# Performance work log

Hardware: AMD Instinct MI355X
Metric: run time of the kernel (lower is better)

Reference implementation:

```python
import jax, jax.numpy as jnp
import numpy as np

B = 2048   # batch
D = 1280   # backbone feature dim (hardcoded in module)
E = 8      # num_classes == number of expert heads
ALPHA = 0.1
EPS = 1e-5


def _bn(x, g, b, m, v):
    # BatchNorm1d in eval mode: running stats
    return (x - m) * jax.lax.rsqrt(v + EPS) * g + b


def _ln(x, g, b):
    mu = jnp.mean(x, axis=-1, keepdims=True)
    var = jnp.mean((x - mu) ** 2, axis=-1, keepdims=True)
    return (x - mu) * jax.lax.rsqrt(var + EPS) * g + b


@jax.custom_vjp
def _grad_reverse(x):
    return x

def _gr_fwd(x):
    return x, None

def _gr_bwd(_, g):
    return (-ALPHA * g,)

_grad_reverse.defvjp(_gr_fwd, _gr_bwd)


def setup_inputs() -> dict:
    key = jax.random.key(0)
    ks = iter(jax.random.split(key, 80))
    def w(*s):
        return jax.random.normal(next(ks), s, dtype=jnp.float32) * 0.02
    def u(*s):
        return jax.random.uniform(next(ks), s, dtype=jnp.float32) + 0.5
    inp = {"source": jax.random.normal(next(ks), (B, D), dtype=jnp.float32)}
    # bottleneck: Linear(1280,512)+BN+ReLU, Linear(512,256)+BN+ReLU
    inp.update(bw1=w(D, 512), bb1=jnp.zeros(512), bg1=jnp.ones(512), bbe1=jnp.zeros(512), bm1=w(512), bv1=u(512))
    inp.update(bw2=w(512, 256), bb2=jnp.zeros(256), bg2=jnp.ones(256), bbe2=jnp.zeros(256), bm2=w(256), bv2=u(256))
    # source_fc: Linear(256, E) + LogSoftmax
    inp.update(cw=w(256, E), cb=jnp.zeros(E))
    # domain classifier: 1280->1024->1024->512->2 with BN
    inp.update(dw1=w(D, 1024), db1=jnp.zeros(1024), dg1=jnp.ones(1024), dbe1=jnp.zeros(1024), dm1=w(1024), dv1=u(1024))
    inp.update(dw2=w(1024, 1024), db2=jnp.zeros(1024), dg2=jnp.ones(1024), dbe2=jnp.zeros(1024), dm2=w(1024), dv2=u(1024))
    inp.update(dw3=w(1024, 512), db3=jnp.zeros(512), dg3=jnp.ones(512), dbe3=jnp.zeros(512), dm3=w(512), dv3=u(512))
    inp.update(dw4=w(512, 2), db4=jnp.zeros(2))
    # E stacked expert MLPs: 1280->1024->1024->512->2 with LayerNorm
    inp.update(ew1=w(E, D, 1024), eb1=jnp.zeros((E, 1024)), eg1=jnp.ones((E, 1024)), ebe1=jnp.zeros((E, 1024)))
    inp.update(ew2=w(E, 1024, 1024), eb2=jnp.zeros((E, 1024)), eg2=jnp.ones((E, 1024)), ebe2=jnp.zeros((E, 1024)))
    inp.update(ew3=w(E, 1024, 512), eb3=jnp.zeros((E, 512)), eg3=jnp.ones((E, 512)), ebe3=jnp.zeros((E, 512)))
    inp.update(ew4=w(E, 512, 2), eb4=jnp.zeros((E, 2)))
    return inp


def reference(source, bw1, bb1, bg1, bbe1, bm1, bv1, bw2, bb2, bg2, bbe2, bm2, bv2, cw, cb,
              dw1, db1, dg1, dbe1, dm1, dv1, dw2, db2, dg2, dbe2, dm2, dv2,
              dw3, db3, dg3, dbe3, dm3, dv3, dw4, db4,
              ew1, eb1, eg1, ebe1, ew2, eb2, eg2, ebe2, ew3, eb3, eg3, ebe3, ew4, eb4):
    share = source  # sharedNet modeled as identity on extracted features
    # bottleneck + classifier head
    h = jax.nn.relu(_bn(share @ bw1 + bb1, bg1, bbe1, bm1, bv1))
    h = jax.nn.relu(_bn(h @ bw2 + bb2, bg2, bbe2, bm2, bv2))
    src = jax.nn.log_softmax(h @ cw + cb, axis=-1)            # [B, E]
    label = jnp.argmax(src, axis=-1)                          # routing labels (detached by argmax)
    # gradient-reversed features
    rev = _grad_reverse(share)
    # global domain classifier (dropout = identity in eval)
    d = jax.nn.relu(_bn(rev @ dw1 + db1, dg1, dbe1, dm1, dv1))
    d = jax.nn.relu(_bn(d @ dw2 + db2, dg2, dbe2, dm2, dv2))
    d = jax.nn.relu(_bn(d @ dw3 + db3, dg3, dbe3, dm3, dv3))
    dclf = jax.nn.log_softmax(d @ dw4 + db4, axis=-1)         # [B, 2]
    # per-class domain experts: dense all-expert compute + per-sample gather
    x = jax.nn.relu(_ln(jnp.einsum('bd,edh->beh', rev, ew1) + eb1[None], eg1[None], ebe1[None]))
    x = jax.nn.relu(_ln(jnp.einsum('beh,ehk->bek', x, ew2) + eb2[None], eg2[None], ebe2[None]))
    x = jax.nn.relu(_ln(jnp.einsum('beh,ehk->bek', x, ew3) + eb3[None], eg3[None], ebe3[None]))
    eo = jax.nn.log_softmax(jnp.einsum('beh,ehk->bek', x, ew4) + eb4[None], axis=-1)  # [B, E, 2]
    sout = jnp.take_along_axis(eo, label[:, None, None], axis=1)[:, 0, :]             # [B, 2]
    return (src, dclf, sout, share)
```

## Files before the change

kernel.cpp:

```cpp
#include <hip/hip_runtime.h>

typedef unsigned short u16;
typedef short s8v __attribute__((ext_vector_type(8)));
typedef float f4v __attribute__((ext_vector_type(4)));

#define AS1 __attribute__((address_space(1)))
#define AS3 __attribute__((address_space(3)))

__device__ __forceinline__ float bf2f(u16 u) {
    union { unsigned int i; float f; } x; x.i = ((unsigned int)u) << 16; return x.f;
}
__device__ __forceinline__ u16 f2bf(float f) {
    union { float f; unsigned int i; } x; x.f = f;
    unsigned int r = x.i + 0x7fffu + ((x.i >> 16) & 1u);
    return (u16)(r >> 16);
}

__device__ __forceinline__ void glds16(const u16* g, u16* l) {
    __builtin_amdgcn_global_load_lds((AS1 void*)(g), (AS3 void*)(l), 16, 0, 0);
}

__device__ __forceinline__ int swz(int row, int kq) {
    return row * 64 + ((((kq >> 3) ^ row) & 7) << 3);
}

__global__ __launch_bounds__(256) void convT2_k(const float* __restrict__ Wa,
        const float* __restrict__ Wb, int zSplit,
        u16* __restrict__ WT, int N, int K)
{
    const int z = blockIdx.z;
    const float* W = (z < zSplit) ? Wa + (size_t)z * K * N
                                  : Wb + (size_t)(z - zSplit) * K * N;
    WT += (size_t)z * K * N;
    const int n0 = blockIdx.x * 64, k0 = blockIdx.y * 64;
    __shared__ float t[64][65];
    const int r = threadIdx.x >> 2;
    const int c = (threadIdx.x & 3) << 4;
    const float* wp = W + (size_t)(k0 + r) * N + n0 + c;
    #pragma unroll
    for (int q = 0; q < 16; q += 4) {
        float4 f = *(const float4*)(wp + q);
        t[c + q + 0][r] = f.x; t[c + q + 1][r] = f.y;
        t[c + q + 2][r] = f.z; t[c + q + 3][r] = f.w;
    }
    __syncthreads();
    u16* op = WT + (size_t)(n0 + r) * K + k0 + c;
    #pragma unroll
    for (int q = 0; q < 16; q += 8) {
        s8v v;
        #pragma unroll
        for (int j = 0; j < 8; ++j) v[j] = (short)f2bf(t[r][c + q + j]);
        *(s8v*)(op + q) = v;
    }
}

__global__ __launch_bounds__(256) void conv_k(const float* __restrict__ in,
        u16* __restrict__ out, int n8)
{
    const int i = blockIdx.x * 256 + threadIdx.x;
    if (i >= n8) return;
    const float4 f0 = ((const float4*)in)[i * 2];
    const float4 f1 = ((const float4*)in)[i * 2 + 1];
    s8v v;
    v[0]=(short)f2bf(f0.x); v[1]=(short)f2bf(f0.y);
    v[2]=(short)f2bf(f0.z); v[3]=(short)f2bf(f0.w);
    v[4]=(short)f2bf(f1.x); v[5]=(short)f2bf(f1.y);
    v[6]=(short)f2bf(f1.z); v[7]=(short)f2bf(f1.w);
    ((s8v*)out)[i] = v;
}

__device__ __forceinline__ void stage_tile(u16* AsH, u16* BsH,
        const u16* ga, const u16* gb, int kk, int ldsq, int K)
{
    #pragma unroll
    for (int q = 0; q < 4; ++q) {
        glds16(ga + kk + (size_t)q * 32 * K, AsH + q * 2048 + ldsq);
        glds16(gb + kk + (size_t)q * 32 * K, BsH + q * 2048 + ldsq);
    }
}

template<int HASDOM>
__global__ __launch_bounds__(256) void gemm_bt128_k(
    const u16* __restrict__ A0, size_t aStrideZ,
    const u16* __restrict__ WT0,
    const float* __restrict__ ebias,
    const float* __restrict__ dbias, const float* __restrict__ dgam,
    const float* __restrict__ dbet,  const float* __restrict__ dmean,
    const float* __restrict__ dvar,  int zdom,
    u16* __restrict__ out0, int M, int N, int K)
{
    const int z = blockIdx.z;
    const u16* A  = A0  + (size_t)z * aStrideZ;
    const u16* WT = WT0 + (size_t)z * N * K;
    u16* out = out0 + (size_t)z * M * N;

    const int n0 = blockIdx.x * 128, m0 = blockIdx.y * 128;
    const int t = threadIdx.x;
    const int w = t >> 6, lane = t & 63;
    const int lq = lane >> 4, lr = lane & 15;
    const int wm = (w >> 1) * 64, wn = (w & 1) * 64;

    __shared__ __align__(16) u16 As[2 * 128 * 64];
    __shared__ __align__(16) u16 Bs[2 * 128 * 64];

    f4v acc[4][4] = {};

    const int schunk = ((t & 7) ^ ((t >> 3) & 7)) << 3;
    const u16* ga = A  + (size_t)(m0 + (t >> 3)) * K + schunk;
    const u16* gb = WT + (size_t)(n0 + (t >> 3)) * K + schunk;
    const int ldsq = w * 512;

    const int NT = K >> 6;
    int cur = 0;
    stage_tile(As, Bs, ga, gb, 0, ldsq, K);
    __syncthreads();

    for (int tk = 0; tk < NT; ++tk) {
        if (tk + 1 < NT)
            stage_tile(As + (cur ^ 1) * 8192, Bs + (cur ^ 1) * 8192,
                       ga, gb, (tk + 1) << 6, ldsq, K);
        const u16* Ah = As + cur * 8192;
        const u16* Bh = Bs + cur * 8192;
        __builtin_amdgcn_s_setprio(1);
        #pragma unroll
        for (int ks = 0; ks < 64; ks += 32) {
            const int kq = ks + (lq << 3);
            s8v a[4], b[4];
            #pragma unroll
            for (int i = 0; i < 4; ++i) a[i] = *(const s8v*)&Ah[swz(wm + i*16 + lr, kq)];
            #pragma unroll
            for (int j = 0; j < 4; ++j) b[j] = *(const s8v*)&Bh[swz(wn + j*16 + lr, kq)];
            #pragma unroll
            for (int i = 0; i < 4; ++i)
                #pragma unroll
                for (int j = 0; j < 4; ++j)
                    acc[i][j] = __builtin_amdgcn_mfma_f32_16x16x32_bf16(a[i], b[j], acc[i][j], 0, 0, 0);
        }
        __builtin_amdgcn_s_setprio(0);
        __syncthreads();
        cur ^= 1;
    }

    float scale[4], shift[4];
    const bool dom = HASDOM && (z == zdom);
    #pragma unroll
    for (int j = 0; j < 4; ++j) {
        const int c = n0 + wn + j * 16 + lr;
        if (dom) {
            const float s = dgam[c] / sqrtf(dvar[c] + 1e-5f);
            scale[j] = s;
            shift[j] = (dbias[c] - dmean[c]) * s + dbet[c];
        } else {
            scale[j] = 1.f;
            shift[j] = ebias[(size_t)z * N + c];
        }
    }
    const int r0 = lq << 2;
    #pragma unroll
    for (int i = 0; i < 4; ++i) {
        #pragma unroll
        for (int r = 0; r < 4; ++r) {
            const int grow = m0 + wm + i * 16 + r0 + r;
            u16* orow = out + (size_t)grow * N + n0 + wn + lr;
            #pragma unroll
            for (int j = 0; j < 4; ++j) {
                float y = fmaf(acc[i][j][r], scale[j], shift[j]);
                if (dom) y = fmaxf(y, 0.f);
                orow[j * 16] = f2bf(y);
            }
        }
    }
}

__global__ __launch_bounds__(256) void gemm_f32sk_k(
    const float* __restrict__ A, const float* __restrict__ W,
    float* __restrict__ out, int M, int N, int K, int Ks)
{
    const int n0 = blockIdx.x * 64, m0 = blockIdx.y * 64;
    const int kb = blockIdx.z * Ks;
    out += (size_t)blockIdx.z * M * N;
    const int tid = threadIdx.x;
    const int tx = tid & 15, ty = tid >> 4;
    __shared__ float As[64][65];
    __shared__ float Bs[64][64];
    float acc[4][4] = {};
    const int sr = tid >> 2;
    const int sc = (tid & 3) << 4;
    for (int kk = kb; kk < kb + Ks; kk += 64) {
        const float* ap = A + (size_t)(m0 + sr) * K + kk + sc;
        #pragma unroll
        for (int q = 0; q < 4; ++q) {
            float4 f = *(const float4*)(ap + q * 4);
            As[sr][sc + q*4 + 0] = f.x; As[sr][sc + q*4 + 1] = f.y;
            As[sr][sc + q*4 + 2] = f.z; As[sr][sc + q*4 + 3] = f.w;
        }
        const float* wp = W + (size_t)(kk + sr) * N + n0 + sc;
        #pragma unroll
        for (int q = 0; q < 4; ++q)
            *(float4*)&Bs[sr][sc + q*4] = *(const float4*)(wp + q * 4);
        __syncthreads();
        #pragma unroll 4
        for (int kq = 0; kq < 64; ++kq) {
            float a[4], bv[4];
            #pragma unroll
            for (int i = 0; i < 4; ++i) a[i] = As[ty*4 + i][kq];
            #pragma unroll
            for (int j = 0; j < 4; ++j) bv[j] = Bs[kq][tx*4 + j];
            #pragma unroll
            for (int i = 0; i < 4; ++i)
                #pragma unroll
                for (int j = 0; j < 4; ++j)
                    acc[i][j] = fmaf(a[i], bv[j], acc[i][j]);
        }
        __syncthreads();
    }
    #pragma unroll
    for (int j = 0; j < 4; ++j) {
        const int c = n0 + tx*4 + j;
        #pragma unroll
        for (int i = 0; i < 4; ++i)
            out[(size_t)(m0 + ty*4 + i) * N + c] = acc[i][j];
    }
}

__global__ __launch_bounds__(256) void h2cls_k(
    const float* __restrict__ hp,
    const float* __restrict__ bb1, const float* __restrict__ bg1,
    const float* __restrict__ bbe1, const float* __restrict__ bm1,
    const float* __restrict__ bv1,
    const float* __restrict__ bw2, const float* __restrict__ bb2,
    const float* __restrict__ bg2, const float* __restrict__ bbe2,
    const float* __restrict__ bm2, const float* __restrict__ bv2,
    const float* __restrict__ cw,  const float* __restrict__ cb,
    float* __restrict__ out_src, int* __restrict__ label, int B)
{
    const int b0 = blockIdx.x * 4;
    const int t = threadIdx.x;
    const size_t sl = (size_t)B * 512;
    __shared__ float h1s[4][512];
    __shared__ float h2s[4][256];

    #pragma unroll
    for (int cc = 0; cc < 2; ++cc) {
        const int c = t + cc * 256;
        const float sc = bg1[c] / sqrtf(bv1[c] + 1e-5f);
        const float sh = (bb1[c] - bm1[c]) * sc + bbe1[c];
        #pragma unroll
        for (int s = 0; s < 4; ++s) {
            const size_t ix = (size_t)(b0 + s) * 512 + c;
            const float v = hp[ix] + hp[ix + sl] + hp[ix + 2*sl] + hp[ix + 3*sl];
            h1s[s][c] = fmaxf(fmaf(v, sc, sh), 0.f);
        }
    }
    __syncthreads();

    float acc[4] = {};
    #pragma unroll 4
    for (int k = 0; k < 512; ++k) {
        const float wv = bw2[(size_t)k * 256 + t];
        #pragma unroll
        for (int s = 0; s < 4; ++s) acc[s] = fmaf(h1s[s][k], wv, acc[s]);
    }
    const float sc2 = bg2[t] / sqrtf(bv2[t] + 1e-5f);
    const float sh2 = (bb2[t] - bm2[t]) * sc2 + bbe2[t];
    #pragma unroll
    for (int s = 0; s < 4; ++s) h2s[s][t] = fmaxf(fmaf(acc[s], sc2, sh2), 0.f);
    __syncthreads();

    const int s = t >> 6, lane = t & 63;
    float p[8] = {};
    for (int k = lane; k < 256; k += 64) {
        const float x = h2s[s][k];
        #pragma unroll
        for (int c = 0; c < 8; ++c) p[c] = fmaf(x, cw[k * 8 + c], p[c]);
    }
    #pragma unroll
    for (int off = 32; off; off >>= 1)
        #pragma unroll
        for (int c = 0; c < 8; ++c) p[c] += __shfl_xor(p[c], off, 64);
    if (lane == 0) {
        const int b = b0 + s;
        float lg[8];
        #pragma unroll
        for (int c = 0; c < 8; ++c) lg[c] = p[c] + cb[c];
        float mx = lg[0]; int am = 0;
        #pragma unroll
        for (int c = 1; c < 8; ++c) if (lg[c] > mx) { mx = lg[c]; am = c; }
        float ssum = 0.f;
        #pragma unroll
        for (int c = 0; c < 8; ++c) ssum += expf(lg[c] - mx);
        const float lse = mx + logf(ssum);
        #pragma unroll
        for (int c = 0; c < 8; ++c) out_src[b * 8 + c] = lg[c] - lse;
        label[b] = am;
    }
}

template<int N>
__global__ __launch_bounds__(256) void ln_relu_k(u16* __restrict__ Y,
        const float* __restrict__ g, const float* __restrict__ bb)
{
    const int z = blockIdx.y;
    u16* y = Y + ((size_t)z * gridDim.x + blockIdx.x) * N;
    const float* gz = g  + (size_t)z * N;
    const float* bz = bb + (size_t)z * N;
    const int t = threadIdx.x;
    constexpr int C = N >> 8;
    float vals[C];
    if (C == 4) {
        ushort4 u = ((const ushort4*)y)[t];
        vals[0] = bf2f(u.x); vals[1] = bf2f(u.y);
        vals[2] = bf2f(u.z); vals[3] = bf2f(u.w);
    } else {
        ushort2 u = ((const ushort2*)y)[t];
        vals[0] = bf2f(u.x); vals[1] = bf2f(u.y);
    }
    float s = 0.f, sq = 0.f;
    #pragma unroll
    for (int i = 0; i < C; ++i) { s += vals[i]; sq += vals[i] * vals[i]; }
    #pragma unroll
    for (int off = 32; off; off >>= 1) {
        s  += __shfl_xor(s,  off, 64);
        sq += __shfl_xor(sq, off, 64);
    }
    __shared__ float rs[4], rq[4];
    if ((t & 63) == 0) { rs[t >> 6] = s; rq[t >> 6] = sq; }
    __syncthreads();
    s  = rs[0] + rs[1] + rs[2] + rs[3];
    sq = rq[0] + rq[1] + rq[2] + rq[3];
    const float inv = 1.f / (float)N;
    const float mu  = s * inv;
    const float var = sq * inv - mu * mu;
    const float rstd = rsqrtf(var + 1e-5f);
    if (C == 4) {
        float4 gv = ((const float4*)gz)[t];
        float4 bv = ((const float4*)bz)[t];
        ushort4 o;
        o.x = f2bf(fmaxf((vals[0] - mu) * rstd * gv.x + bv.x, 0.f));
        o.y = f2bf(fmaxf((vals[1] - mu) * rstd * gv.y + bv.y, 0.f));
        o.z = f2bf(fmaxf((vals[2] - mu) * rstd * gv.z + bv.z, 0.f));
        o.w = f2bf(fmaxf((vals[3] - mu) * rstd * gv.w + bv.w, 0.f));
        ((ushort4*)y)[t] = o;
    } else {
        float2 gv = ((const float2*)gz)[t];
        float2 bv = ((const float2*)bz)[t];
        ushort2 o;
        o.x = f2bf(fmaxf((vals[0] - mu) * rstd * gv.x + bv.x, 0.f));
        o.y = f2bf(fmaxf((vals[1] - mu) * rstd * gv.y + bv.y, 0.f));
        ((ushort2*)y)[t] = o;
    }
}

__global__ __launch_bounds__(64) void head2_k(const u16* __restrict__ X, size_t xsz,
        const float* __restrict__ W, size_t wsz,
        const float* __restrict__ bias, size_t bsz,
        int K, float* __restrict__ out, size_t osz)
{
    const int b = blockIdx.x, z = blockIdx.y;
    const int lane = threadIdx.x;
    const u16* x = X + z * xsz + (size_t)b * K;
    const float* Wz = W + z * wsz;
    const float* bz = bias + z * bsz;
    float* o = out + z * osz + (size_t)b * 2;
    float p0 = 0.f, p1 = 0.f;
    for (int k = lane; k < K; k += 64) {
        const float xv = bf2f(x[k]);
        p0 = fmaf(xv, Wz[k * 2],     p0);
        p1 = fmaf(xv, Wz[k * 2 + 1], p1);
    }
    #pragma unroll
    for (int off = 32; off; off >>= 1) {
        p0 += __shfl_xor(p0, off, 64);
        p1 += __shfl_xor(p1, off, 64);
    }
    if (lane == 0) {
        const float l0 = p0 + bz[0];
        const float l1 = p1 + bz[1];
        const float mx = fmaxf(l0, l1);
        const float lse = mx + logf(expf(l0 - mx) + expf(l1 - mx));
        o[0] = l0 - lse;
        o[1] = l1 - lse;
    }
}

__global__ __launch_bounds__(256) void gather_k(const float* __restrict__ eo,
        const int* __restrict__ label, float* __restrict__ out, int B)
{
    const int b = blockIdx.x * 256 + threadIdx.x;
    if (b >= B) return;
    const int e = label[b];
    out[b * 2]     = eo[((size_t)e * B + b) * 2];
    out[b * 2 + 1] = eo[((size_t)e * B + b) * 2 + 1];
}

__global__ __launch_bounds__(256) void copy16_k(const uint4* __restrict__ in,
                                                uint4* __restrict__ out, int n16)
{
    const int i = blockIdx.x * blockDim.x + threadIdx.x;
    if (i < n16) out[i] = in[i];
}


extern "C" void kernel_launch(void* const* d_in, const int* in_sizes, int n_in,
                              void* d_out, int out_size, void* d_ws, size_t ws_size,
                              hipStream_t stream)
{
    const int B = 2048, D = 1280, E = 8;

    const float* src = (const float*)d_in[0];
    const float *bw1 = (const float*)d_in[1],  *bb1 = (const float*)d_in[2],
                *bg1 = (const float*)d_in[3],  *bbe1 = (const float*)d_in[4],
                *bm1 = (const float*)d_in[5],  *bv1 = (const float*)d_in[6];
    const float *bw2 = (const float*)d_in[7],  *bb2 = (const float*)d_in[8],
                *bg2 = (const float*)d_in[9],  *bbe2 = (const float*)d_in[10],
                *bm2 = (const float*)d_in[11], *bv2 = (const float*)d_in[12];
    const float *cw  = (const float*)d_in[13], *cb  = (const float*)d_in[14];
    const float *dw1 = (const float*)d_in[15], *db1 = (const float*)d_in[16],
                *dg1 = (const float*)d_in[17], *dbe1 = (const float*)d_in[18],
                *dm1 = (const float*)d_in[19], *dv1 = (const float*)d_in[20];
    const float *dw2 = (const float*)d_in[21], *db2 = (const float*)d_in[22],
                *dg2 = (const float*)d_in[23], *dbe2 = (const float*)d_in[24],
                *dm2 = (const float*)d_in[25], *dv2 = (const float*)d_in[26];
    const float *dw3 = (const float*)d_in[27], *db3 = (const float*)d_in[28],
                *dg3 = (const float*)d_in[29], *dbe3 = (const float*)d_in[30],
                *dm3 = (const float*)d_in[31], *dv3 = (const float*)d_in[32];
    const float *dw4 = (const float*)d_in[33], *db4 = (const float*)d_in[34];
    const float *ew1 = (const float*)d_in[35], *eb1 = (const float*)d_in[36],
                *eg1 = (const float*)d_in[37], *ebe1 = (const float*)d_in[38];
    const float *ew2 = (const float*)d_in[39], *eb2 = (const float*)d_in[40],
                *eg2 = (const float*)d_in[41], *ebe2 = (const float*)d_in[42];
    const float *ew3 = (const float*)d_in[43], *eb3 = (const float*)d_in[44],
                *eg3 = (const float*)d_in[45], *ebe3 = (const float*)d_in[46];
    const float *ew4 = (const float*)d_in[47], *eb4 = (const float*)d_in[48];

    float* out_src   = (float*)d_out;
    float* out_dclf  = out_src + B * E;
    float* out_sout  = out_dclf + B * 2;
    float* out_share = out_sout + B * 2;

    char* ws = (char*)d_ws;
    u16*   wslot = (u16*)ws;
    u16*   srcb  = (u16*)(ws + 13107200);
    u16*   acta  = (u16*)(ws + 18350080);
    u16*   actb  = (u16*)(ws + 39321600);
    float* eo    = (float*)(ws + 60293120);
    int*   label = (int*)(ws + 60424192);
    float* hp    = (float*)(ws + 18350080);

    const size_t s1024 = (size_t)B * 1024, s512 = (size_t)B * 512;

    conv_k<<<dim3(B * D / 8 / 256), 256, 0, stream>>>(src, srcb, B * D / 8);
    copy16_k<<<dim3(B * D * 4 / 16 / 256), 256, 0, stream>>>(
        (const uint4*)src, (uint4*)out_share, B * D * 4 / 16);

    gemm_f32sk_k<<<dim3(512 / 64, B / 64, 4), 256, 0, stream>>>(
        src, bw1, hp, B, 512, D, 320);
    h2cls_k<<<dim3(B / 4), 256, 0, stream>>>(
        hp, bb1, bg1, bbe1, bm1, bv1, bw2, bb2, bg2, bbe2, bm2, bv2,
        cw, cb, out_src, label, B);

    convT2_k<<<dim3(16, 20, 5), 256, 0, stream>>>(ew1, dw1, 4, wslot, 1024, 1280);
    gemm_bt128_k<1><<<dim3(8, 16, 5), 256, 0, stream>>>(
        srcb, 0, wslot, eb1, db1, dg1, dbe1, dm1, dv1, 4, acta, B, 1024, 1280);
    ln_relu_k<1024><<<dim3(B, 4), 256, 0, stream>>>(acta, eg1, ebe1);

    convT2_k<<<dim3(16, 16, 5), 256, 0, stream>>>(ew2, dw2, 4, wslot, 1024, 1024);
    gemm_bt128_k<1><<<dim3(8, 16, 5), 256, 0, stream>>>(
        acta, s1024, wslot, eb2, db2, dg2, dbe2, dm2, dv2, 4, actb, B, 1024, 1024);
    ln_relu_k<1024><<<dim3(B, 4), 256, 0, stream>>>(actb, eg2, ebe2);

    convT2_k<<<dim3(8, 16, 5), 256, 0, stream>>>(ew3, dw3, 4, wslot, 512, 1024);
    gemm_bt128_k<1><<<dim3(4, 16, 5), 256, 0, stream>>>(
        actb, s1024, wslot, eb3, db3, dg3, dbe3, dm3, dv3, 4, acta, B, 512, 1024);
    ln_relu_k<512><<<dim3(B, 4), 256, 0, stream>>>(acta, eg3, ebe3);

    head2_k<<<dim3(B, 4), 64, 0, stream>>>(
        acta, s512, ew4, 1024, eb4, 2, 512, eo, (size_t)B * 2);
    head2_k<<<dim3(B, 1), 64, 0, stream>>>(
        acta + (size_t)4 * B * 512, 0, dw4, 0, db4, 0, 512, out_dclf, 0);

    convT2_k<<<dim3(16, 20, 4), 256, 0, stream>>>(
        ew1 + (size_t)4*1280*1024, ew1 + (size_t)4*1280*1024, 4, wslot, 1024, 1280);
    gemm_bt128_k<0><<<dim3(8, 16, 4), 256, 0, stream>>>(
        srcb, 0, wslot, eb1 + (size_t)4*1024,
        nullptr, nullptr, nullptr, nullptr, nullptr, -1, acta, B, 1024, 1280);
    ln_relu_k<1024><<<dim3(B, 4), 256, 0, stream>>>(acta, eg1 + (size_t)4*1024, ebe1 + (size_t)4*1024);

    convT2_k<<<dim3(16, 16, 4), 256, 0, stream>>>(
        ew2 + (size_t)4*1024*1024, ew2 + (size_t)4*1024*1024, 4, wslot, 1024, 1024);
    gemm_bt128_k<0><<<dim3(8, 16, 4), 256, 0, stream>>>(
        acta, s1024, wslot, eb2 + (size_t)4*1024,
        nullptr, nullptr, nullptr, nullptr, nullptr, -1, actb, B, 1024, 1024);
    ln_relu_k<1024><<<dim3(B, 4), 256, 0, stream>>>(actb, eg2 + (size_t)4*1024, ebe2 + (size_t)4*1024);

    convT2_k<<<dim3(8, 16, 4), 256, 0, stream>>>(
        ew3 + (size_t)4*1024*512, ew3 + (size_t)4*1024*512, 4, wslot, 512, 1024);
    gemm_bt128_k<0><<<dim3(4, 16, 4), 256, 0, stream>>>(
        actb, s1024, wslot, eb3 + (size_t)4*512,
        nullptr, nullptr, nullptr, nullptr, nullptr, -1, acta, B, 512, 1024);
    ln_relu_k<512><<<dim3(B, 4), 256, 0, stream>>>(acta, eg3 + (size_t)4*512, ebe3 + (size_t)4*512);

    head2_k<<<dim3(B, 4), 64, 0, stream>>>(
        acta, s512, ew4 + (size_t)4*512*2, 1024, eb4 + 8, 2, 512,
        eo + (size_t)4 * B * 2, (size_t)B * 2);

    gather_k<<<dim3(B / 256), 256, 0, stream>>>(eo, label, out_sout, B);
}
```

Baseline: 620.9 us.

## Split bottleneck layer-2 into tiled split-K GEMM plus classifier kernel; vectorize head loads

The fused h2cls kernel, which ran the 512->256 bottleneck matmul with only 4 rows per block, is replaced by three kernels. A tiny kernel precomputes the BN1 scale and shift. A 64x64 tiled split-K GEMM applies BN1+ReLU while staging activations into shared memory, which gives far more weight reuse. A classifier kernel reduces the split-K partials, applies BN2+ReLU and computes log-softmax/argmax. The expert head kernel also loads activations and weights with 16-byte vector loads; the cost is two extra launches and a partial-sum buffer round trip through global memory.

```diff
diff --git a/kernel.cpp b/kernel.cpp
--- a/kernel.cpp
+++ b/kernel.cpp
@@ -223,63 +223,125 @@
     }
 }
 
-__global__ __launch_bounds__(256) void h2cls_k(
-    const float* __restrict__ hp,
-    const float* __restrict__ bb1, const float* __restrict__ bg1,
-    const float* __restrict__ bbe1, const float* __restrict__ bm1,
-    const float* __restrict__ bv1,
-    const float* __restrict__ bw2, const float* __restrict__ bb2,
+__global__ __launch_bounds__(256) void bnpre_k(const float* __restrict__ g,
+        const float* __restrict__ be, const float* __restrict__ bb,
+        const float* __restrict__ m, const float* __restrict__ v,
+        float* __restrict__ scs, float* __restrict__ shs, int N)
+{
+    const int k = blockIdx.x * 256 + threadIdx.x;
+    if (k >= N) return;
+    const float sc = g[k] / sqrtf(v[k] + 1e-5f);
+    scs[k] = sc;
+    shs[k] = (bb[k] - m[k]) * sc + be[k];
+}
+
+__global__ __launch_bounds__(256) void h2gemm_k(
+    const float* __restrict__ hp, const float* __restrict__ scs,
+    const float* __restrict__ shs, const float* __restrict__ bw2,
+    float* __restrict__ out, int B)
+{
+    const int n0 = blockIdx.x * 64, m0 = blockIdx.y * 64;
+    const int kb = blockIdx.z * 128;
+    out += (size_t)blockIdx.z * B * 256;
+    const size_t sl = (size_t)B * 512;
+    const int tid = threadIdx.x;
+    const int tx = tid & 15, ty = tid >> 4;
+    __shared__ float As[64][65];
+    __shared__ float Bs[64][64];
+    float acc[4][4] = {};
+    const int sr = tid >> 2;
+    const int sc = (tid & 3) << 4;
+    for (int kk = kb; kk < kb + 128; kk += 64) {
+        const float* ap = hp + (size_t)(m0 + sr) * 512 + kk + sc;
+        #pragma unroll
+        for (int q = 0; q < 4; ++q) {
+            const float4 f0 = *(const float4*)(ap + q * 4);
+            const float4 f1 = *(const float4*)(ap + sl + q * 4);
+            const float4 f2 = *(const float4*)(ap + 2 * sl + q * 4);
+            const float4 f3 = *(const float4*)(ap + 3 * sl + q * 4);
+            const float4 g = *(const float4*)(scs + kk + sc + q * 4);
+            const float4 h = *(const float4*)(shs + kk + sc + q * 4);
+            As[sr][sc + q*4 + 0] = fmaxf(fmaf(f0.x + f1.x + f2.x + f3.x, g.x, h.x), 0.f);
+            As[sr][sc + q*4 + 1] = fmaxf(fmaf(f0.y + f1.y + f2.y + f3.y, g.y, h.y), 0.f);
+            As[sr][sc + q*4 + 2] = fmaxf(fmaf(f0.z + f1.z + f2.z + f3.z, g.z, h.z), 0.f);
+            As[sr][sc + q*4 + 3] = fmaxf(fmaf(f0.w + f1.w + f2.w + f3.w, g.w, h.w), 0.f);
+        }
+        const float* wp = bw2 + (size_t)(kk + sr) * 256 + n0 + sc;
+        #pragma unroll
+        for (int q = 0; q < 4; ++q)
+            *(float4*)&Bs[sr][sc + q*4] = *(const float4*)(wp + q * 4);
+        __syncthreads();
+        #pragma unroll 4
+        for (int kq = 0; kq < 64; ++kq) {
+            float a[4], bv[4];
+            #pragma unroll
+            for (int i = 0; i < 4; ++i) a[i] = As[ty*4 + i][kq];
+            #pragma unroll
+            for (int j = 0; j < 4; ++j) bv[j] = Bs[kq][tx*4 + j];
+            #pragma unroll
+            for (int i = 0; i < 4; ++i)
+                #pragma unroll
+                for (int j = 0; j < 4; ++j)
+                    acc[i][j] = fmaf(a[i], bv[j], acc[i][j]);
+        }
+        __syncthreads();
+    }
+    #pragma unroll
+    for (int j = 0; j < 4; ++j) {
+        const int c = n0 + tx*4 + j;
+        #pragma unroll
+        for (int i = 0; i < 4; ++i)
+            out[(size_t)(m0 + ty*4 + i) * 256 + c] = acc[i][j];
+    }
+}
+
+__global__ __launch_bounds__(256) void cls_k(
+    const float* __restrict__ h2p,
     const float* __restrict__ bg2, const float* __restrict__ bbe2,
-    const float* __restrict__ bm2, const float* __restrict__ bv2,
+    const float* __restrict__ bb2, const float* __restrict__ bm2,
+    const float* __restrict__ bv2,
     const float* __restrict__ cw,  const float* __restrict__ cb,
     float* __restrict__ out_src, int* __restrict__ label, int B)
 {
-    const int b0 = blockIdx.x * 4;
-    const int t = threadIdx.x;
-    const size_t sl = (size_t)B * 512;
-    __shared__ float h1s[4][512];
-    __shared__ float h2s[4][256];
-
-    #pragma unroll
-    for (int cc = 0; cc < 2; ++cc) {
-        const int c = t + cc * 256;
-        const float sc = bg1[c] / sqrtf(bv1[c] + 1e-5f);
-        const float sh = (bb1[c] - bm1[c]) * sc + bbe1[c];
-        #pragma unroll
-        for (int s = 0; s < 4; ++s) {
-            const size_t ix = (size_t)(b0 + s) * 512 + c;
-            const float v = hp[ix] + hp[ix + sl] + hp[ix + 2*sl] + hp[ix + 3*sl];
-            h1s[s][c] = fmaxf(fmaf(v, sc, sh), 0.f);
-        }
-    }
-    __syncthreads();
-
-    float acc[4] = {};
-    #pragma unroll 4
-    for (int k = 0; k < 512; ++k) {
-        const float wv = bw2[(size_t)k * 256 + t];
-        #pragma unroll
-        for (int s = 0; s < 4; ++s) acc[s] = fmaf(h1s[s][k], wv, acc[s]);
-    }
-    const float sc2 = bg2[t] / sqrtf(bv2[t] + 1e-5f);
-    const float sh2 = (bb2[t] - bm2[t]) * sc2 + bbe2[t];
-    #pragma unroll
-    for (int s = 0; s < 4; ++s) h2s[s][t] = fmaxf(fmaf(acc[s], sc2, sh2), 0.f);
-    __syncthreads();
-
-    const int s = t >> 6, lane = t & 63;
+    const int b = blockIdx.x * 4 + (threadIdx.x >> 6);
+    const int lane = threadIdx.x & 63;
+    const size_t sl = (size_t)B * 256;
+    const float* hb = h2p + (size_t)b * 256 + lane * 4;
+    const float4 v0 = *(const float4*)(hb);
+    const float4 v1 = *(const float4*)(hb + sl);
+    const float4 v2 = *(const float4*)(hb + 2 * sl);
+    const float4 v3 = *(const float4*)(hb + 3 * sl);
+    const float4 gv = ((const float4*)bg2)[lane];
+    const float4 vv = ((const float4*)bv2)[lane];
+    const float4 bbv = ((const float4*)bb2)[lane];
+    const float4 bmv = ((const float4*)bm2)[lane];
+    const float4 bev = ((const float4*)bbe2)[lane];
+    float h[4];
+    {
+        const float s0 = gv.x / sqrtf(vv.x + 1e-5f);
+        const float s1 = gv.y / sqrtf(vv.y + 1e-5f);
+        const float s2 = gv.z / sqrtf(vv.z + 1e-5f);
+        const float s3 = gv.w / sqrtf(vv.w + 1e-5f);
+        h[0] = fmaxf(fmaf(v0.x + v1.x + v2.x + v3.x, s0, (bbv.x - bmv.x) * s0 + bev.x), 0.f);
+        h[1] = fmaxf(fmaf(v0.y + v1.y + v2.y + v3.y, s1, (bbv.y - bmv.y) * s1 + bev.y), 0.f);
+        h[2] = fmaxf(fmaf(v0.z + v1.z + v2.z + v3.z, s2, (bbv.z - bmv.z) * s2 + bev.z), 0.f);
+        h[3] = fmaxf(fmaf(v0.w + v1.w + v2.w + v3.w, s3, (bbv.w - bmv.w) * s3 + bev.w), 0.f);
+    }
     float p[8] = {};
-    for (int k = lane; k < 256; k += 64) {
-        const float x = h2s[s][k];
-        #pragma unroll
-        for (int c = 0; c < 8; ++c) p[c] = fmaf(x, cw[k * 8 + c], p[c]);
+    #pragma unroll
+    for (int j = 0; j < 4; ++j) {
+        const float4 c0 = ((const float4*)cw)[(lane * 4 + j) * 2];
+        const float4 c1 = ((const float4*)cw)[(lane * 4 + j) * 2 + 1];
+        p[0] = fmaf(h[j], c0.x, p[0]); p[1] = fmaf(h[j], c0.y, p[1]);
+        p[2] = fmaf(h[j], c0.z, p[2]); p[3] = fmaf(h[j], c0.w, p[3]);
+        p[4] = fmaf(h[j], c1.x, p[4]); p[5] = fmaf(h[j], c1.y, p[5]);
+        p[6] = fmaf(h[j], c1.z, p[6]); p[7] = fmaf(h[j], c1.w, p[7]);
     }
     #pragma unroll
     for (int off = 32; off; off >>= 1)
         #pragma unroll
         for (int c = 0; c < 8; ++c) p[c] += __shfl_xor(p[c], off, 64);
     if (lane == 0) {
-        const int b = b0 + s;
         float lg[8];
         #pragma unroll
         for (int c = 0; c < 8; ++c) lg[c] = p[c] + cb[c];
@@ -363,10 +425,21 @@
     const float* bz = bias + z * bsz;
     float* o = out + z * osz + (size_t)b * 2;
     float p0 = 0.f, p1 = 0.f;
-    for (int k = lane; k < K; k += 64) {
-        const float xv = bf2f(x[k]);
-        p0 = fmaf(xv, Wz[k * 2],     p0);
-        p1 = fmaf(xv, Wz[k * 2 + 1], p1);
+    for (int k8 = lane; k8 < (K >> 3); k8 += 64) {
+        const uint4 raw = ((const uint4*)x)[k8];
+        const u16* pu = (const u16*)&raw;
+        const float4 w0 = ((const float4*)Wz)[k8 * 4 + 0];
+        const float4 w1 = ((const float4*)Wz)[k8 * 4 + 1];
+        const float4 w2 = ((const float4*)Wz)[k8 * 4 + 2];
+        const float4 w3 = ((const float4*)Wz)[k8 * 4 + 3];
+        p0 = fmaf(bf2f(pu[0]), w0.x, p0); p1 = fmaf(bf2f(pu[0]), w0.y, p1);
+        p0 = fmaf(bf2f(pu[1]), w0.z, p0); p1 = fmaf(bf2f(pu[1]), w0.w, p1);
+        p0 = fmaf(bf2f(pu[2]), w1.x, p0); p1 = fmaf(bf2f(pu[2]), w1.y, p1);
+        p0 = fmaf(bf2f(pu[3]), w1.z, p0); p1 = fmaf(bf2f(pu[3]), w1.w, p1);
+        p0 = fmaf(bf2f(pu[4]), w2.x, p0); p1 = fmaf(bf2f(pu[4]), w2.y, p1);
+        p0 = fmaf(bf2f(pu[5]), w2.z, p0); p1 = fmaf(bf2f(pu[5]), w2.w, p1);
+        p0 = fmaf(bf2f(pu[6]), w3.x, p0); p1 = fmaf(bf2f(pu[6]), w3.y, p1);
+        p0 = fmaf(bf2f(pu[7]), w3.z, p0); p1 = fmaf(bf2f(pu[7]), w3.w, p1);
     }
     #pragma unroll
     for (int off = 32; off; off >>= 1) {
@@ -446,6 +519,9 @@
     float* eo    = (float*)(ws + 60293120);
     int*   label = (int*)(ws + 60424192);
     float* hp    = (float*)(ws + 18350080);
+    float* h2p   = (float*)(ws);
+    float* scs   = (float*)(ws + 12582912);
+    float* shs   = (float*)(ws + 12587008);
 
     const size_t s1024 = (size_t)B * 1024, s512 = (size_t)B * 512;
 
@@ -453,11 +529,13 @@
     copy16_k<<<dim3(B * D * 4 / 16 / 256), 256, 0, stream>>>(
         (const uint4*)src, (uint4*)out_share, B * D * 4 / 16);
 
+    bnpre_k<<<dim3(2), 256, 0, stream>>>(bg1, bbe1, bb1, bm1, bv1, scs, shs, 512);
     gemm_f32sk_k<<<dim3(512 / 64, B / 64, 4), 256, 0, stream>>>(
         src, bw1, hp, B, 512, D, 320);
-    h2cls_k<<<dim3(B / 4), 256, 0, stream>>>(
-        hp, bb1, bg1, bbe1, bm1, bv1, bw2, bb2, bg2, bbe2, bm2, bv2,
-        cw, cb, out_src, label, B);
+    h2gemm_k<<<dim3(256 / 64, B / 64, 4), 256, 0, stream>>>(
+        hp, scs, shs, bw2, h2p, B);
+    cls_k<<<dim3(B / 4), 256, 0, stream>>>(
+        h2p, bg2, bbe2, bb2, bm2, bv2, cw, cb, out_src, label, B);
 
     convT2_k<<<dim3(16, 20, 5), 256, 0, stream>>>(ew1, dw1, 4, wslot, 1024, 1280);
     gemm_bt128_k<1><<<dim3(8, 16, 5), 256, 0, stream>>>(
```

Measured after the change: 582.8 us. 6.1% less time.
